# Performance work log

Hardware: AMD Instinct MI355X
Metric: run time of the kernel (lower is better)

The kernel has to match this reference:

```python
import jax, jax.numpy as jnp
import numpy as np

DIM = 512
HEADS = 8


def setup_inputs() -> dict:
    key = jax.random.key(0)
    ks = jax.random.split(key, 8)
    B, N_mm, N_a, N_v = 2, 64, 256, 256
    xmm = jax.random.normal(ks[0], (B, N_mm, DIM), dtype=jnp.float32)
    xa = jax.random.normal(ks[1], (B, N_a, DIM), dtype=jnp.float32)
    xv = jax.random.normal(ks[2], (B, N_v, DIM), dtype=jnp.float32)
    # Learned params (torch nn.Linear stores weight as [out, in]); qkv_bias=False, proj has bias.
    Wq = jax.random.normal(ks[3], (DIM, DIM), dtype=jnp.float32) * 0.02
    Wkv = jax.random.normal(ks[4], (2 * DIM, 2 * DIM), dtype=jnp.float32) * 0.02
    Wproj = jax.random.normal(ks[5], (DIM, DIM), dtype=jnp.float32) * 0.02
    bproj = jnp.zeros((DIM,), dtype=jnp.float32)
    return {"xmm": xmm, "xa": xa, "xv": xv, "Wq": Wq, "Wkv": Wkv, "Wproj": Wproj, "bproj": bproj}


def reference(xmm, xa, xv, Wq, Wkv, Wproj, bproj):
    B, N_mm, dim = xmm.shape
    N_v, N_a = xv.shape[1], xa.shape[1]
    H = HEADS
    hd = dim // H
    scale = hd ** (-0.5)

    # q: [B, H, N_mm, hd]
    q = (xmm @ Wq.T).reshape(B, N_mm, H, hd).transpose(0, 2, 1, 3)

    # kv(x_va) where x_va[b,i,j] = concat(xv[b,i], xa[b,j]); since kv is linear,
    # kv(x_va) = xv @ Wkv[:, :dim].T + xa @ Wkv[:, dim:].T, broadcast over the cartesian grid.
    pv = xv @ Wkv[:, :dim].T   # [B, N_v, 2*dim]
    pa = xa @ Wkv[:, dim:].T   # [B, N_a, 2*dim]
    kv = (pv[:, :, None, :] + pa[:, None, :, :]).reshape(B, N_v * N_a, 2, H, hd)
    k = kv[:, :, 0].transpose(0, 2, 1, 3)  # [B, H, N_v*N_a, hd]
    v = kv[:, :, 1].transpose(0, 2, 1, 3)  # [B, H, N_v*N_a, hd]

    attn = jax.nn.softmax(jnp.einsum('bhqd,bhkd->bhqk', q, k) * scale, axis=-1)
    out = jnp.einsum('bhqk,bhkd->bhqd', attn, v)          # [B, H, N_mm, hd]
    out = out.transpose(0, 2, 1, 3).reshape(B, N_mm, dim)  # [B, N_mm, dim]
    return out @ Wproj.T + bproj
```

## Files before the change

### kernel.cpp

```cpp
#include <hip/hip_runtime.h>


#define OQ   0
#define OKP  65536
#define OVT  589824
#define SIDESZ 262144
#define OHOUT16 1114112

typedef _Float16 f16x8 __attribute__((ext_vector_type(8)));
typedef _Float16 f16x4 __attribute__((ext_vector_type(4)));
typedef float f32x4 __attribute__((ext_vector_type(4)));

__device__ __forceinline__ void stage_tile_f16(
    const float* __restrict__ g, int ld, int base, int k0,
    _Float16* __restrict__ lds, int sr, int sq)
{
  const float* p = &g[(size_t)(base + sr) * ld + k0 + sq * 16];
  float4 v0 = *reinterpret_cast<const float4*>(p);
  float4 v1 = *reinterpret_cast<const float4*>(p + 4);
  float4 v2 = *reinterpret_cast<const float4*>(p + 8);
  float4 v3 = *reinterpret_cast<const float4*>(p + 12);
  f16x8 h0 = {(_Float16)v0.x, (_Float16)v0.y, (_Float16)v0.z, (_Float16)v0.w,
              (_Float16)v1.x, (_Float16)v1.y, (_Float16)v1.z, (_Float16)v1.w};
  f16x8 h1 = {(_Float16)v2.x, (_Float16)v2.y, (_Float16)v2.z, (_Float16)v2.w,
              (_Float16)v3.x, (_Float16)v3.y, (_Float16)v3.z, (_Float16)v3.w};
  int c0 = (sq * 2) ^ (sr & 7);
  int c1 = (sq * 2 + 1) ^ (sr & 7);
  *reinterpret_cast<f16x8*>(&lds[sr * 64 + c0 * 8]) = h0;
  *reinterpret_cast<f16x8*>(&lds[sr * 64 + c1 * 8]) = h1;
}

template <int MODE>
__device__ __forceinline__ void mfma_gemm64(
    const float* __restrict__ A, int lda,
    const float* __restrict__ W, int ldw,
    int bm, int bn, int side,
    _Float16* __restrict__ ws16,
    float* __restrict__ Cf, int ldc, const float* __restrict__ bias)
{
  __shared__ _Float16 As[64 * 64];
  __shared__ _Float16 Ws[64 * 64];
  const int tid = threadIdx.x;
  const int lane = tid & 63;
  const int w = tid >> 6;
  const int wm = w >> 1, wn = w & 1;
  const int sr = tid >> 2;
  const int sq = tid & 3;

  f32x4 acc[2][2] = {};
  const int cl = lane & 15;
  const int kg = lane >> 4;

  for (int k0 = 0; k0 < 512; k0 += 64) {
    __syncthreads();
    stage_tile_f16(A, lda, bm, k0, As, sr, sq);
    stage_tile_f16(W, ldw, bn, k0, Ws, sr, sq);
    __syncthreads();
    #pragma unroll
    for (int ks = 0; ks < 2; ++ks) {
      f16x8 af[2], bf[2];
      #pragma unroll
      for (int mi = 0; mi < 2; ++mi) {
        int row = wm * 32 + mi * 16 + cl;
        int ch = (ks * 4 + kg) ^ (row & 7);
        af[mi] = *reinterpret_cast<const f16x8*>(&As[row * 64 + ch * 8]);
      }
      #pragma unroll
      for (int ni = 0; ni < 2; ++ni) {
        int col = wn * 32 + ni * 16 + cl;
        int ch = (ks * 4 + kg) ^ (col & 7);
        bf[ni] = *reinterpret_cast<const f16x8*>(&Ws[col * 64 + ch * 8]);
      }
      #pragma unroll
      for (int mi = 0; mi < 2; ++mi)
        #pragma unroll
        for (int ni = 0; ni < 2; ++ni)
          acc[mi][ni] = __builtin_amdgcn_mfma_f32_16x16x32_f16(
              af[mi], bf[ni], acc[mi][ni], 0, 0, 0);
    }
  }

  #pragma unroll
  for (int mi = 0; mi < 2; ++mi) {
    #pragma unroll
    for (int ni = 0; ni < 2; ++ni) {
      int row0 = bm + wm * 32 + mi * 16 + kg * 4;
      int col = bn + wn * 32 + ni * 16 + cl;
      if (MODE == 0) {
        _Float16* dst = ws16 + OQ + (size_t)row0 * 512 + col;
        #pragma unroll
        for (int r = 0; r < 4; ++r)
          dst[(size_t)r * 512] = (_Float16)(acc[mi][ni][r] * 0.125f);
      } else if (MODE == 1) {
        if (col < 512) {
          _Float16* dst = ws16 + OKP + (size_t)side * SIDESZ + (size_t)row0 * 512 + col;
          #pragma unroll
          for (int r = 0; r < 4; ++r)
            dst[(size_t)r * 512] = (_Float16)acc[mi][ni][r];
        } else {
          _Float16* dst = ws16 + OVT + (size_t)side * SIDESZ +
                          (size_t)(col - 512) * 512 + row0;
          f16x4 v = {(_Float16)acc[mi][ni][0], (_Float16)acc[mi][ni][1],
                     (_Float16)acc[mi][ni][2], (_Float16)acc[mi][ni][3]};
          *reinterpret_cast<f16x4*>(dst) = v;
        }
      } else {
        float bv = bias ? bias[col] : 0.f;
        #pragma unroll
        for (int r = 0; r < 4; ++r)
          Cf[(size_t)(row0 + r) * ldc + col] = acc[mi][ni][r] + bv;
      }
    }
  }
}

__global__ __launch_bounds__(256) void fused_proj_kernel(
    const float* __restrict__ xmm, const float* __restrict__ xa,
    const float* __restrict__ xv, const float* __restrict__ Wq,
    const float* __restrict__ Wkv, _Float16* __restrict__ ws16)
{
  const int id = blockIdx.x;
  if (id < 16) {
    mfma_gemm64<0>(xmm, 512, Wq, 512, (id >> 3) * 64, (id & 7) * 64, 0,
                   ws16, nullptr, 0, nullptr);
  } else if (id < 144) {
    int t = id - 16;
    mfma_gemm64<1>(xv, 512, Wkv, 1024, (t >> 4) * 64, (t & 15) * 64, 0,
                   ws16, nullptr, 0, nullptr);
  } else {
    int t = id - 144;
    mfma_gemm64<1>(xa, 512, Wkv + 512, 1024, (t >> 4) * 64, (t & 15) * 64, 1,
                   ws16, nullptr, 0, nullptr);
  }
}

__global__ __launch_bounds__(256) void proj_out_kernel(
    const _Float16* __restrict__ ws16, const float* __restrict__ Wproj,
    const float* __restrict__ bproj, float* __restrict__ out)
{
  const float* hout = (const float*)(ws16 + OHOUT16);
  mfma_gemm64<2>(hout, 512, Wproj, 512,
                 (int)(blockIdx.x >> 3) * 64, (int)(blockIdx.x & 7) * 64, 0,
                 nullptr, out, 512, bproj);
}

__global__ __launch_bounds__(256) void attn_kernel(
    const _Float16* __restrict__ ws16, float* __restrict__ hout)
{
  __shared__ _Float16 P_lds[4][16][256];
  float* mbuf = reinterpret_cast<float*>(&P_lds[0][0][0]);

  const int bh = blockIdx.x >> 1;
  const int qh = blockIdx.x & 1;
  const int b = bh >> 3, h = bh & 7;

  const int tid = threadIdx.x;
  const int w = tid >> 6;
  const int lane = tid & 63;
  const int side = w & 1;
  const int qtl = w >> 1;
  const int q0 = qh * 32 + qtl * 16;
  const int l15 = lane & 15;
  const int g = lane >> 4;

  const _Float16* Kg = ws16 + OKP + (size_t)side * SIDESZ;
  const _Float16* VTg = ws16 + OVT + (size_t)side * SIDESZ;

  f16x8 qb[2];
  #pragma unroll
  for (int ks = 0; ks < 2; ++ks)
    qb[ks] = *reinterpret_cast<const f16x8*>(
        &ws16[OQ + (size_t)(b * 64 + q0 + l15) * 512 + h * 64 + ks * 32 + g * 8]);

  f32x4 st[16] = {};
  #pragma unroll
  for (int f = 0; f < 16; ++f) {
    #pragma unroll
    for (int ks = 0; ks < 2; ++ks) {
      f16x8 af = *reinterpret_cast<const f16x8*>(
          &Kg[(size_t)(b * 256 + f * 16 + l15) * 512 + h * 64 + ks * 32 + g * 8]);
      st[f] = __builtin_amdgcn_mfma_f32_16x16x32_f16(af, qb[ks], st[f], 0, 0, 0);
    }
  }

  float m = st[0][0];
  #pragma unroll
  for (int f = 0; f < 16; ++f)
    #pragma unroll
    for (int r = 0; r < 4; ++r) m = fmaxf(m, st[f][r]);
  m = fmaxf(m, __shfl_xor(m, 16));
  m = fmaxf(m, __shfl_xor(m, 32));
  float lsum = 0.f;
  #pragma unroll
  for (int f = 0; f < 16; ++f)
    #pragma unroll
    for (int r = 0; r < 4; ++r) {
      float e = __expf(st[f][r] - m);
      st[f][r] = e;
      lsum += e;
    }
  lsum += __shfl_xor(lsum, 16);
  lsum += __shfl_xor(lsum, 32);

  #pragma unroll
  for (int f = 0; f < 16; ++f) {
    f16x4 pk = {(_Float16)st[f][0], (_Float16)st[f][1],
                (_Float16)st[f][2], (_Float16)st[f][3]};
    int chunk = 2 * f + (g >> 1);
    int swz = chunk ^ (l15 & 7);
    *reinterpret_cast<f16x4*>(&P_lds[w][l15][swz * 8 + (g & 1) * 4]) = pk;
  }
  __syncthreads();

  f32x4 oc[4] = {};
  #pragma unroll
  for (int ks = 0; ks < 8; ++ks) {
    f16x8 pa = *reinterpret_cast<const f16x8*>(
        &P_lds[w][l15][((4 * ks + g) ^ (l15 & 7)) * 8]);
    #pragma unroll
    for (int nf = 0; nf < 4; ++nf) {
      f16x8 vb = *reinterpret_cast<const f16x8*>(
          &VTg[(size_t)(h * 64 + nf * 16 + l15) * 512 + b * 256 + ks * 32 + g * 8]);
      oc[nf] = __builtin_amdgcn_mfma_f32_16x16x32_f16(pa, vb, oc[nf], 0, 0, 0);
    }
  }
  __syncthreads();

  #pragma unroll
  for (int nf = 0; nf < 4; ++nf)
    #pragma unroll
    for (int r = 0; r < 4; ++r)
      mbuf[((size_t)side * 32 + qtl * 16 + 4 * g + r) * 68 + nf * 16 + l15] =
          oc[nf][r];
  if (g == 0)
    mbuf[((size_t)side * 32 + qtl * 16 + l15) * 68 + 64] = lsum;
  __syncthreads();

  {
    int q = tid >> 3, d0 = (tid & 7) * 8;
    const float* rv = &mbuf[(size_t)q * 68];
    const float* ra = &mbuf[(size_t)(32 + q) * 68];
    float invv = 1.0f / rv[64];
    float inva = 1.0f / ra[64];
    float4 o0, o1;
    const float4 v0 = *reinterpret_cast<const float4*>(rv + d0);
    const float4 v1 = *reinterpret_cast<const float4*>(rv + d0 + 4);
    const float4 a0 = *reinterpret_cast<const float4*>(ra + d0);
    const float4 a1 = *reinterpret_cast<const float4*>(ra + d0 + 4);
    o0.x = v0.x * invv + a0.x * inva; o0.y = v0.y * invv + a0.y * inva;
    o0.z = v0.z * invv + a0.z * inva; o0.w = v0.w * invv + a0.w * inva;
    o1.x = v1.x * invv + a1.x * inva; o1.y = v1.y * invv + a1.y * inva;
    o1.z = v1.z * invv + a1.z * inva; o1.w = v1.w * invv + a1.w * inva;
    float* dst = &hout[(size_t)(b * 64 + qh * 32 + q) * 512 + h * 64 + d0];
    *reinterpret_cast<float4*>(dst) = o0;
    *reinterpret_cast<float4*>(dst + 4) = o1;
  }
}

extern "C" void kernel_launch(void* const* d_in, const int* in_sizes, int n_in,
                              void* d_out, int out_size, void* d_ws, size_t ws_size,
                              hipStream_t stream) {
  const float* xmm   = (const float*)d_in[0];
  const float* xa    = (const float*)d_in[1];
  const float* xv    = (const float*)d_in[2];
  const float* Wq    = (const float*)d_in[3];
  const float* Wkv   = (const float*)d_in[4];
  const float* Wproj = (const float*)d_in[5];
  const float* bproj = (const float*)d_in[6];
  float* out = (float*)d_out;
  _Float16* ws16 = (_Float16*)d_ws;
  float* hout = (float*)(ws16 + OHOUT16);

  fused_proj_kernel<<<272, 256, 0, stream>>>(xmm, xa, xv, Wq, Wkv, ws16);
  attn_kernel<<<32, 256, 0, stream>>>(ws16, hout);
  proj_out_kernel<<<16, 256, 0, stream>>>(ws16, Wproj, bproj, out);
}
```

Baseline: 40.44 us.

## Split attention across 128 blocks with head-major K/V layout and deferred side merge

The Q/K/V projections now write head-major contiguous slabs, so each attention block reads compact per-head tiles instead of strided rows. The attention kernel goes from 32 to 128 blocks: each block handles one side and a 16-query tile. The four waves split keys and combine the softmax max and sum through shared memory, and each wave computes 16 output columns. The two sides are written to separate buffers and summed while the output projection stages its A tile, which removes the in-kernel merge but adds an extra fp32 buffer read in the last GEMM.

```diff
diff --git a/kernel.cpp b/kernel.cpp
--- a/kernel.cpp
+++ b/kernel.cpp
@@ -1,9 +1,9 @@
 #include <hip/hip_runtime.h>
 
 
-#define OQ   0
-#define OKP  65536
-#define OVT  589824
+#define OQ16   0
+#define OK16   65536
+#define OVT16  589824
 #define SIDESZ 262144
 #define OHOUT16 1114112
 
@@ -12,14 +12,25 @@
 typedef float f32x4 __attribute__((ext_vector_type(4)));
 
 __device__ __forceinline__ void stage_tile_f16(
-    const float* __restrict__ g, int ld, int base, int k0,
-    _Float16* __restrict__ lds, int sr, int sq)
+    const float* __restrict__ g, const float* __restrict__ g2, int ld,
+    int base, int k0, _Float16* __restrict__ lds, int sr, int sq)
 {
   const float* p = &g[(size_t)(base + sr) * ld + k0 + sq * 16];
   float4 v0 = *reinterpret_cast<const float4*>(p);
   float4 v1 = *reinterpret_cast<const float4*>(p + 4);
   float4 v2 = *reinterpret_cast<const float4*>(p + 8);
   float4 v3 = *reinterpret_cast<const float4*>(p + 12);
+  if (g2) {
+    const float* p2 = &g2[(size_t)(base + sr) * ld + k0 + sq * 16];
+    float4 u0 = *reinterpret_cast<const float4*>(p2);
+    float4 u1 = *reinterpret_cast<const float4*>(p2 + 4);
+    float4 u2 = *reinterpret_cast<const float4*>(p2 + 8);
+    float4 u3 = *reinterpret_cast<const float4*>(p2 + 12);
+    v0.x += u0.x; v0.y += u0.y; v0.z += u0.z; v0.w += u0.w;
+    v1.x += u1.x; v1.y += u1.y; v1.z += u1.z; v1.w += u1.w;
+    v2.x += u2.x; v2.y += u2.y; v2.z += u2.z; v2.w += u2.w;
+    v3.x += u3.x; v3.y += u3.y; v3.z += u3.z; v3.w += u3.w;
+  }
   f16x8 h0 = {(_Float16)v0.x, (_Float16)v0.y, (_Float16)v0.z, (_Float16)v0.w,
               (_Float16)v1.x, (_Float16)v1.y, (_Float16)v1.z, (_Float16)v1.w};
   f16x8 h1 = {(_Float16)v2.x, (_Float16)v2.y, (_Float16)v2.z, (_Float16)v2.w,
@@ -32,7 +43,7 @@
 
 template <int MODE>
 __device__ __forceinline__ void mfma_gemm64(
-    const float* __restrict__ A, int lda,
+    const float* __restrict__ A, const float* __restrict__ A2, int lda,
     const float* __restrict__ W, int ldw,
     int bm, int bn, int side,
     _Float16* __restrict__ ws16,
@@ -53,8 +64,8 @@
 
   for (int k0 = 0; k0 < 512; k0 += 64) {
     __syncthreads();
-    stage_tile_f16(A, lda, bm, k0, As, sr, sq);
-    stage_tile_f16(W, ldw, bn, k0, Ws, sr, sq);
+    stage_tile_f16(A, A2, lda, bm, k0, As, sr, sq);
+    stage_tile_f16(W, nullptr, ldw, bn, k0, Ws, sr, sq);
     __syncthreads();
     #pragma unroll
     for (int ks = 0; ks < 2; ++ks) {
@@ -87,19 +98,25 @@
       int row0 = bm + wm * 32 + mi * 16 + kg * 4;
       int col = bn + wn * 32 + ni * 16 + cl;
       if (MODE == 0) {
-        _Float16* dst = ws16 + OQ + (size_t)row0 * 512 + col;
+        int b = row0 >> 6, n = row0 & 63, h = col >> 6, d = col & 63;
+        _Float16* dst = ws16 + OQ16 + (((size_t)b * 8 + h) * 64 + n) * 64 + d;
         #pragma unroll
         for (int r = 0; r < 4; ++r)
-          dst[(size_t)r * 512] = (_Float16)(acc[mi][ni][r] * 0.125f);
+          dst[(size_t)r * 64] = (_Float16)(acc[mi][ni][r] * 0.125f);
       } else if (MODE == 1) {
+        int b = row0 >> 8, key = row0 & 255;
         if (col < 512) {
-          _Float16* dst = ws16 + OKP + (size_t)side * SIDESZ + (size_t)row0 * 512 + col;
+          int h = col >> 6, d = col & 63;
+          _Float16* dst = ws16 + OK16 + (size_t)side * SIDESZ +
+                          (((size_t)b * 8 + h) * 256 + key) * 64 + d;
           #pragma unroll
           for (int r = 0; r < 4; ++r)
-            dst[(size_t)r * 512] = (_Float16)acc[mi][ni][r];
+            dst[(size_t)r * 64] = (_Float16)acc[mi][ni][r];
         } else {
-          _Float16* dst = ws16 + OVT + (size_t)side * SIDESZ +
-                          (size_t)(col - 512) * 512 + row0;
+          int dp = col - 512;
+          int h = dp >> 6, d = dp & 63;
+          _Float16* dst = ws16 + OVT16 + (size_t)side * SIDESZ +
+                          (((size_t)b * 8 + h) * 64 + d) * 256 + key;
           f16x4 v = {(_Float16)acc[mi][ni][0], (_Float16)acc[mi][ni][1],
                      (_Float16)acc[mi][ni][2], (_Float16)acc[mi][ni][3]};
           *reinterpret_cast<f16x4*>(dst) = v;
@@ -121,16 +138,16 @@
 {
   const int id = blockIdx.x;
   if (id < 16) {
-    mfma_gemm64<0>(xmm, 512, Wq, 512, (id >> 3) * 64, (id & 7) * 64, 0,
-                   ws16, nullptr, 0, nullptr);
+    mfma_gemm64<0>(xmm, nullptr, 512, Wq, 512, (id >> 3) * 64, (id & 7) * 64,
+                   0, ws16, nullptr, 0, nullptr);
   } else if (id < 144) {
     int t = id - 16;
-    mfma_gemm64<1>(xv, 512, Wkv, 1024, (t >> 4) * 64, (t & 15) * 64, 0,
-                   ws16, nullptr, 0, nullptr);
+    mfma_gemm64<1>(xv, nullptr, 512, Wkv, 1024, (t >> 4) * 64, (t & 15) * 64,
+                   0, ws16, nullptr, 0, nullptr);
   } else {
     int t = id - 144;
-    mfma_gemm64<1>(xa, 512, Wkv + 512, 1024, (t >> 4) * 64, (t & 15) * 64, 1,
-                   ws16, nullptr, 0, nullptr);
+    mfma_gemm64<1>(xa, nullptr, 512, Wkv + 512, 1024, (t >> 4) * 64,
+                   (t & 15) * 64, 1, ws16, nullptr, 0, nullptr);
   }
 }
 
@@ -138,122 +155,112 @@
     const _Float16* __restrict__ ws16, const float* __restrict__ Wproj,
     const float* __restrict__ bproj, float* __restrict__ out)
 {
-  const float* hout = (const float*)(ws16 + OHOUT16);
-  mfma_gemm64<2>(hout, 512, Wproj, 512,
+  const float* hv = (const float*)(ws16 + OHOUT16);
+  const float* ha = hv + 65536;
+  mfma_gemm64<2>(hv, ha, 512, Wproj, 512,
                  (int)(blockIdx.x >> 3) * 64, (int)(blockIdx.x & 7) * 64, 0,
                  nullptr, out, 512, bproj);
 }
 
 __global__ __launch_bounds__(256) void attn_kernel(
-    const _Float16* __restrict__ ws16, float* __restrict__ hout)
-{
-  __shared__ _Float16 P_lds[4][16][256];
-  float* mbuf = reinterpret_cast<float*>(&P_lds[0][0][0]);
-
-  const int bh = blockIdx.x >> 1;
-  const int qh = blockIdx.x & 1;
-  const int b = bh >> 3, h = bh & 7;
+    const _Float16* __restrict__ ws16, float* __restrict__ hv,
+    float* __restrict__ ha)
+{
+  __shared__ _Float16 P_lds[16][256];
+  __shared__ float m_s[4][16];
+  __shared__ float l_s[4][16];
+
+  const int x = blockIdx.x;
+  const int side = x & 1;
+  const int qtl = (x >> 1) & 3;
+  const int bh = x >> 3;
+  const int b = bh >> 3;
 
   const int tid = threadIdx.x;
   const int w = tid >> 6;
   const int lane = tid & 63;
-  const int side = w & 1;
-  const int qtl = w >> 1;
-  const int q0 = qh * 32 + qtl * 16;
   const int l15 = lane & 15;
   const int g = lane >> 4;
 
-  const _Float16* Kg = ws16 + OKP + (size_t)side * SIDESZ;
-  const _Float16* VTg = ws16 + OVT + (size_t)side * SIDESZ;
+  const _Float16* slabQ = ws16 + OQ16 + (size_t)bh * 4096;
+  const _Float16* slabK = ws16 + OK16 + (size_t)side * SIDESZ + (size_t)bh * 16384;
+  const _Float16* slabV = ws16 + OVT16 + (size_t)side * SIDESZ + (size_t)bh * 16384;
 
   f16x8 qb[2];
   #pragma unroll
   for (int ks = 0; ks < 2; ++ks)
     qb[ks] = *reinterpret_cast<const f16x8*>(
-        &ws16[OQ + (size_t)(b * 64 + q0 + l15) * 512 + h * 64 + ks * 32 + g * 8]);
-
-  f32x4 st[16] = {};
-  #pragma unroll
-  for (int f = 0; f < 16; ++f) {
+        &slabQ[(size_t)(qtl * 16 + l15) * 64 + ks * 32 + g * 8]);
+
+  f32x4 st[4] = {};
+  #pragma unroll
+  for (int f = 0; f < 4; ++f) {
     #pragma unroll
     for (int ks = 0; ks < 2; ++ks) {
       f16x8 af = *reinterpret_cast<const f16x8*>(
-          &Kg[(size_t)(b * 256 + f * 16 + l15) * 512 + h * 64 + ks * 32 + g * 8]);
+          &slabK[(size_t)(w * 64 + f * 16 + l15) * 64 + ks * 32 + g * 8]);
       st[f] = __builtin_amdgcn_mfma_f32_16x16x32_f16(af, qb[ks], st[f], 0, 0, 0);
     }
   }
 
   float m = st[0][0];
   #pragma unroll
-  for (int f = 0; f < 16; ++f)
+  for (int f = 0; f < 4; ++f)
     #pragma unroll
     for (int r = 0; r < 4; ++r) m = fmaxf(m, st[f][r]);
   m = fmaxf(m, __shfl_xor(m, 16));
   m = fmaxf(m, __shfl_xor(m, 32));
+  if (g == 0) m_s[w][l15] = m;
+  __syncthreads();
+
+  float M = fmaxf(fmaxf(m_s[0][l15], m_s[1][l15]),
+                  fmaxf(m_s[2][l15], m_s[3][l15]));
   float lsum = 0.f;
   #pragma unroll
-  for (int f = 0; f < 16; ++f)
+  for (int f = 0; f < 4; ++f)
     #pragma unroll
     for (int r = 0; r < 4; ++r) {
-      float e = __expf(st[f][r] - m);
+      float e = __expf(st[f][r] - M);
       st[f][r] = e;
       lsum += e;
     }
   lsum += __shfl_xor(lsum, 16);
   lsum += __shfl_xor(lsum, 32);
-
-  #pragma unroll
-  for (int f = 0; f < 16; ++f) {
+  if (g == 0) l_s[w][l15] = lsum;
+
+  #pragma unroll
+  for (int f = 0; f < 4; ++f) {
     f16x4 pk = {(_Float16)st[f][0], (_Float16)st[f][1],
                 (_Float16)st[f][2], (_Float16)st[f][3]};
-    int chunk = 2 * f + (g >> 1);
+    int chunk = w * 8 + 2 * f + (g >> 1);
     int swz = chunk ^ (l15 & 7);
-    *reinterpret_cast<f16x4*>(&P_lds[w][l15][swz * 8 + (g & 1) * 4]) = pk;
+    *reinterpret_cast<f16x4*>(&P_lds[l15][swz * 8 + (g & 1) * 4]) = pk;
   }
   __syncthreads();
 
-  f32x4 oc[4] = {};
+  f32x4 L4 = {};
+  #pragma unroll
+  for (int w2 = 0; w2 < 4; ++w2) {
+    f32x4 lw = *reinterpret_cast<const f32x4*>(&l_s[w2][g * 4]);
+    L4 += lw;
+  }
+
+  f32x4 oc = {};
   #pragma unroll
   for (int ks = 0; ks < 8; ++ks) {
     f16x8 pa = *reinterpret_cast<const f16x8*>(
-        &P_lds[w][l15][((4 * ks + g) ^ (l15 & 7)) * 8]);
-    #pragma unroll
-    for (int nf = 0; nf < 4; ++nf) {
-      f16x8 vb = *reinterpret_cast<const f16x8*>(
-          &VTg[(size_t)(h * 64 + nf * 16 + l15) * 512 + b * 256 + ks * 32 + g * 8]);
-      oc[nf] = __builtin_amdgcn_mfma_f32_16x16x32_f16(pa, vb, oc[nf], 0, 0, 0);
-    }
-  }
-  __syncthreads();
-
-  #pragma unroll
-  for (int nf = 0; nf < 4; ++nf)
-    #pragma unroll
-    for (int r = 0; r < 4; ++r)
-      mbuf[((size_t)side * 32 + qtl * 16 + 4 * g + r) * 68 + nf * 16 + l15] =
-          oc[nf][r];
-  if (g == 0)
-    mbuf[((size_t)side * 32 + qtl * 16 + l15) * 68 + 64] = lsum;
-  __syncthreads();
-
-  {
-    int q = tid >> 3, d0 = (tid & 7) * 8;
-    const float* rv = &mbuf[(size_t)q * 68];
-    const float* ra = &mbuf[(size_t)(32 + q) * 68];
-    float invv = 1.0f / rv[64];
-    float inva = 1.0f / ra[64];
-    float4 o0, o1;
-    const float4 v0 = *reinterpret_cast<const float4*>(rv + d0);
-    const float4 v1 = *reinterpret_cast<const float4*>(rv + d0 + 4);
-    const float4 a0 = *reinterpret_cast<const float4*>(ra + d0);
-    const float4 a1 = *reinterpret_cast<const float4*>(ra + d0 + 4);
-    o0.x = v0.x * invv + a0.x * inva; o0.y = v0.y * invv + a0.y * inva;
-    o0.z = v0.z * invv + a0.z * inva; o0.w = v0.w * invv + a0.w * inva;
-    o1.x = v1.x * invv + a1.x * inva; o1.y = v1.y * invv + a1.y * inva;
-    o1.z = v1.z * invv + a1.z * inva; o1.w = v1.w * invv + a1.w * inva;
-    float* dst = &hout[(size_t)(b * 64 + qh * 32 + q) * 512 + h * 64 + d0];
-    *reinterpret_cast<float4*>(dst) = o0;
-    *reinterpret_cast<float4*>(dst + 4) = o1;
+        &P_lds[l15][((4 * ks + g) ^ (l15 & 7)) * 8]);
+    f16x8 vb = *reinterpret_cast<const f16x8*>(
+        &slabV[(size_t)(w * 16 + l15) * 256 + ks * 32 + g * 8]);
+    oc = __builtin_amdgcn_mfma_f32_16x16x32_f16(pa, vb, oc, 0, 0, 0);
+  }
+
+  float* houtS = side ? ha : hv;
+  const int h = bh & 7;
+  #pragma unroll
+  for (int r = 0; r < 4; ++r) {
+    houtS[(size_t)(b * 64 + qtl * 16 + 4 * g + r) * 512 +
+          h * 64 + w * 16 + l15] = oc[r] * (1.0f / L4[r]);
   }
 }
 
@@ -269,9 +276,10 @@
   const float* bproj = (const float*)d_in[6];
   float* out = (float*)d_out;
   _Float16* ws16 = (_Float16*)d_ws;
-  float* hout = (float*)(ws16 + OHOUT16);
+  float* hv = (float*)(ws16 + OHOUT16);
+  float* ha = hv + 65536;
 
   fused_proj_kernel<<<272, 256, 0, stream>>>(xmm, xa, xv, Wq, Wkv, ws16);
-  attn_kernel<<<32, 256, 0, stream>>>(ws16, hout);
+  attn_kernel<<<128, 256, 0, stream>>>(ws16, hv, ha);
   proj_out_kernel<<<16, 256, 0, stream>>>(ws16, Wproj, bproj, out);
 }
```

Result: faster. 37.04 us (-8.4%).
